# Optimization experiments

Hardware: AMD Instinct MI355X
Metric: run time of the kernel (lower is better)

The kernel has to match this reference:

```python
import jax, jax.numpy as jnp
import numpy as np

B, L, D, H, N, F_, DM = 16, 2048, 128, 4, 4, 129, 16
DK = D // H
DFF = 2 * D
INT = int(np.sqrt(D))  # 11
V = F_ + 1


def _uinit(key, shape, fan):
    s = float(np.sqrt(6.0 / fan))
    return jax.random.uniform(key, shape, jnp.float32, -s, s)


def setup_inputs() -> dict:
    key = jax.random.key(0)
    ks = jax.random.split(key, 24)
    return {
        "values": jax.random.normal(ks[0], (B, L), jnp.float32),
        "times": jax.random.uniform(ks[1], (B, L), jnp.float32),
        "variables": jax.random.randint(ks[2], (B, L), 0, F_),
        "input_mask": jax.random.randint(ks[3], (B, L), 0, 2).astype(bool),
        "demographics": jax.random.normal(ks[4], (B, DM), jnp.float32),
        # CVE time
        "W1t": _uinit(ks[5], (1, INT), 1 + INT), "b1t": jnp.zeros((INT,), jnp.float32),
        "W2t": _uinit(ks[6], (INT, D), INT + D),
        # CVE value
        "W1v": _uinit(ks[7], (1, INT), 1 + INT), "b1v": jnp.zeros((INT,), jnp.float32),
        "W2v": _uinit(ks[8], (INT, D), INT + D),
        # variable embedding table
        "var_table": jax.random.normal(ks[9], (V, D), jnp.float32),
        # transformer stacks (init_proj: uniform(-s, s), s = sqrt(6/(fan_in+fan_out)) of last two dims)
        "Wq": _uinit(ks[10], (N, H, D, DK), D + DK),
        "Wk": _uinit(ks[11], (N, H, D, DK), D + DK),
        "Wv": _uinit(ks[12], (N, H, D, DK), D + DK),
        "Wo": _uinit(ks[13], (N, D, D), 2 * D),
        "W1": _uinit(ks[14], (N, D, DFF), D + DFF), "b1": jnp.zeros((N, 1, 1, DFF), jnp.float32),
        "W2": _uinit(ks[15], (N, DFF, D), DFF + D), "b2": jnp.zeros((N, 1, 1, D), jnp.float32),
        # fusion attention
        "Wf": _uinit(ks[16], (D, D), 2 * D), "bf": jnp.zeros((D,), jnp.float32),
        "uf": _uinit(ks[17], (D, 1), D + 1),
        # demographics MLP
        "Wd1": _uinit(ks[18], (DM, 2 * D), DM + 2 * D), "bd1": jnp.zeros((2 * D,), jnp.float32),
        "Wd2": _uinit(ks[19], (2 * D, D), 3 * D), "bd2": jnp.zeros((D,), jnp.float32),
        # head: forecast_fc
        "Wh": _uinit(ks[20], (2 * D, F_), 2 * D + F_), "bh": jnp.zeros((F_,), jnp.float32),
    }


def reference(values, times, variables, input_mask, demographics,
              W1t, b1t, W2t, W1v, b1v, W2v, var_table,
              Wq, Wk, Wv, Wo, W1, b1, W2, b2,
              Wf, bf, uf, Wd1, bd1, Wd2, bd2, Wh, bh):
    FMIN = jnp.finfo(values.dtype).min
    # demographics MLP
    demo = jnp.tanh(demographics @ Wd1 + bd1) @ Wd2 + bd2
    # continuous value embeddings (CVE): x -> tanh(x*W1 + b1) @ W2
    te = jnp.tanh(times[..., None] * W1t[0] + b1t) @ W2t    # [B,L,D]
    ve = jnp.tanh(values[..., None] * W1v[0] + b1v) @ W2v   # [B,L,D]
    x = te + ve + var_table[variables]                      # [B,L,D]
    # additive pairwise mask (finite FMIN, matches torch finfo.min semantics)
    m = input_mask
    pair = m[:, :, None] & m[:, None, :]                    # [B,L,L]
    addm = jnp.where(pair[:, None, :, :], 0.0, FMIN)        # [B,1,L,L]
    n_layers = Wq.shape[0]
    bsz, max_len, _ = x.shape
    for i in range(n_layers):
        q = jnp.einsum('bld,hde->bhle', x, Wq[i])
        k = jnp.einsum('bld,hde->bhle', x, Wk[i])
        v = jnp.einsum('bld,hde->bhle', x, Wv[i])
        A = jnp.einsum('bhle,bhke->bhlk', q, k) + addm      # NOTE: no 1/sqrt(dk) scaling, as in source
        A = jax.nn.softmax(A, axis=-1)
        o = jnp.einsum('bhlk,bhke->blhe', A, v).reshape(bsz, max_len, -1)
        x = o @ Wo[i] + x
        f = jax.nn.gelu(x @ W1[i] + b1[i], approximate=False)
        x = f @ W2[i] + b2[i] + x
    # fusion attention pooling
    att = (jnp.tanh(x @ Wf + bf) @ uf)[:, :, 0]             # [B,L]
    att = att + jnp.where(m, 0.0, FMIN)
    w = jax.nn.softmax(att, axis=-1)
    ts = jnp.sum(x * w[:, :, None], axis=1)                 # [B,D]
    emb = jnp.concatenate([ts, demo], axis=-1)              # [B,2D]
    return emb @ Wh + bh                                    # [B,features_num]
```

## Files before the change

### kernel.cpp

```cpp
#include <hip/hip_runtime.h>
#include <hip/hip_bf16.h>
#include <math.h>

#define B_   16
#define L_   2048
#define D_   128
#define H_   4
#define NL_  4
#define DK_  32
#define DFF_ 256
#define INTD_ 11
#define F_OUT 129
#define DM_  16
#define FMINV (-3.402823466e38f)
#define LOG2E 1.4426950408889634f

#define BL_  (B_*L_)
#define SZ_X (BL_*D_)

#define WT_Q 0
#define WT_K 16384
#define WT_V 32768
#define WT_O 49152
#define WT_1 65536
#define WT_2 98304
#define WT_TOT 131072

typedef __attribute__((ext_vector_type(8))) short bf16x8;
typedef __attribute__((ext_vector_type(4))) float f32x4;

#if __has_builtin(__builtin_amdgcn_exp2f)
#define EXP2F(x) __builtin_amdgcn_exp2f(x)
#else
#define EXP2F(x) __expf(0.69314718055994531f*(x))
#endif

static __device__ __forceinline__ short f2bf(float x) {
    union { __hip_bfloat16 h; short s; } u;
    u.h = __float2bfloat16(x);
    return u.s;
}
static __device__ __forceinline__ float bf2f(short s) {
    union { __hip_bfloat16 h; short t; } u;
    u.t = s;
    return __bfloat162float(u.h);
}
static __device__ __forceinline__ void split2(float v, short& h, short& l) {
    h = f2bf(v); l = f2bf(v - bf2f(h));
}
static __device__ __forceinline__ void split_trunc(float v, short& h, short& l) {
    unsigned u = __float_as_uint(v);
    h = (short)(u >> 16);
    float r = v - __uint_as_float(u & 0xffff0000u);
    l = (short)(__float_as_uint(r) >> 16);
}

__global__ __launch_bounds__(256)
void compact_kernel(const int* __restrict__ mask, int* __restrict__ pos,
                    int* __restrict__ kcount, float* __restrict__ cfm,
                    float* __restrict__ x)
{
    int b = blockIdx.x, t = threadIdx.x;
    int lane = t & 63, w = t >> 6;
    __shared__ int wsum[4];
    __shared__ int tot_s;
    int mv[8], loc[8], s = 0;
#pragma unroll
    for (int i = 0; i < 8; ++i) {
        mv[i] = mask[b*L_ + t*8 + i];
        loc[i] = s;
        s += mv[i];
    }
    int v = s;
#pragma unroll
    for (int d = 1; d < 64; d <<= 1) {
        int y = __shfl_up(v, d);
        if (lane >= d) v += y;
    }
    int excl = v - s;
    if (lane == 63) wsum[w] = v;
    __syncthreads();
    int wbase = 0;
    for (int i = 0; i < w; ++i) wbase += wsum[i];
    int base = wbase + excl;
#pragma unroll
    for (int i = 0; i < 8; ++i)
        pos[b*L_ + t*8 + i] = mv[i] ? (base + loc[i]) : -1;
    if (t == 255) { kcount[b] = base + s; tot_s = base + s; }
    __syncthreads();
    int tot = tot_s;
    for (int l = t; l < L_; l += 256) cfm[b*L_ + l] = (l < tot) ? 0.0f : FMINV;
    int end = (tot + 63) & ~63;
    int nz = (end - tot) * D_;
    for (int i = t; i < nz; i += 256)
        x[((size_t)(b*2048 + tot))*D_ + i] = 0.0f;
}

__global__ __launch_bounds__(128)
void embed_kernel(const float* __restrict__ values, const float* __restrict__ times,
                  const int* __restrict__ variables, const int* __restrict__ pos,
                  const float* __restrict__ W1t, const float* __restrict__ b1t,
                  const float* __restrict__ W2t,
                  const float* __restrict__ W1v, const float* __restrict__ b1v,
                  const float* __restrict__ W2v,
                  const float* __restrict__ var_table, float* __restrict__ x)
{
    int bl = blockIdx.x;
// ... 101 lines not shown
#pragma unroll
        for (int j = 0; j < 2; ++j) {
            size_t wi = (size_t)(32*w + 16*j + m)*D_ + 32*ks + 8*qd;
            wh[j] = *(const bf16x8*)(Wh + wi);
            wl[j] = *(const bf16x8*)(Wl + wi);
        }
#pragma unroll
        for (int r4 = 0; r4 < 4; ++r4) {
            bf16x8 ah = *(const bf16x8*)&Ahi[(16*r4 + m)*136 + 32*ks + 8*qd];
            bf16x8 al = *(const bf16x8*)&Alo[(16*r4 + m)*136 + 32*ks + 8*qd];
#pragma unroll
            for (int j = 0; j < 2; ++j) {
                acc[r4][j] = __builtin_amdgcn_mfma_f32_16x16x32_bf16(wh[j], ah, acc[r4][j], 0, 0, 0);
                acc[r4][j] = __builtin_amdgcn_mfma_f32_16x16x32_bf16(wh[j], al, acc[r4][j], 0, 0, 0);
                acc[r4][j] = __builtin_amdgcn_mfma_f32_16x16x32_bf16(wl[j], ah, acc[r4][j], 0, 0, 0);
            }
        }
    }

#pragma unroll
    for (int r4 = 0; r4 < 4; ++r4) {
        int row = row0 + 16*r4 + m;
        int l = row & 2047;
#pragma unroll
        for (int j = 0; j < 2; ++j) {
            int col = 32*w + 16*j + 4*qd;
            f32x4 v = acc[r4][j];
            if (sec == 0) {
                float4 sv = {v[0], v[1], v[2], v[3]};
                *(float4*)(qout + (size_t)row*D_ + col) = sv;
            } else if (sec == 1) {
                size_t idx = ((size_t)((bb*4 + w)*2048 + l))*32 + (col & 31);
                short4 hi4, lo4;
                split2(v[0], hi4.x, lo4.x);
                split2(v[1], hi4.y, lo4.y);
                split2(v[2], hi4.z, lo4.z);
                split2(v[3], hi4.w, lo4.w);
                *(short4*)(khi + idx) = hi4;
                *(short4*)(klo + idx) = lo4;
            } else {
                size_t basep = (size_t)(bb*4 + w)*32;
#pragma unroll
                for (int e = 0; e < 4; ++e) {
                    int d = 16*j + 4*qd + e;
                    short hh, ll; split2(v[e], hh, ll);
                    vhiT[(basep + d)*2048 + l] = hh;
                    vloT[(basep + d)*2048 + l] = ll;
                }
            }
        }
    }
}

__global__ __launch_bounds__(256)
void attn_mfma_kernel(const float* __restrict__ q,
                      const short* __restrict__ khi, const short* __restrict__ klo,
                      const short* __restrict__ vhiT, const short* __restrict__ vloT,
                      const int* __restrict__ kcount, const float* __restrict__ cfm,
                      float* __restrict__ opart, float* __restrict__ mlm,
                      float* __restrict__ mll)
{
    (void)cfm;
    __shared__ short KhiS[2][2048];
    __shared__ short KloS[2][2048];
    __shared__ short Vthi[2][2048];
    __shared__ short Vtlo[2][2048];
    __shared__ short Ps[4][1024];

    const int t    = threadIdx.x;
    const int w    = t >> 6;
    const int lane = t & 63;
    const int m    = lane & 15;
    const int qd   = lane >> 4;
    const int qt = blockIdx.x, b = blockIdx.z;
    const int h = blockIdx.y & 3, half = blockIdx.y >> 2;

    const int Kb = kcount[b];
    if (qt*64 >= Kb) return;
    const int nt = (Kb + 63) >> 6;
    const int ntH = (nt + 1) >> 1;
    const int kt0 = half * ntH;
    const int kt1 = (kt0 + ntH < nt) ? (kt0 + ntH) : nt;
    const size_t mlbase = (((size_t)(b*4 + h))*2 + half)*2048;

    if (kt0 >= kt1) {
        if (lane < 16) {
            mlm[mlbase + qt*64 + 16*w + lane] = FMINV;
            mll[mlbase + qt*64 + 16*w + lane] = 0.0f;
        }
        return;
    }

    const size_t hd = ((size_t)(b*4 + h))*2048*32;
    const int vd = t >> 3;
    const int vk = t & 7;
    const size_t vbase = ((size_t)(b*4 + h)*32 + vd)*2048 + vk*8;
    const int vw_off = vd*64 + ((vk ^ (vd & 7)) << 3);

    const int qrow = qt*64 + 16*w + m;
    const float* qp = q + ((size_t)(b*L_ + qrow))*D_ + h*DK_ + 8*qd;
    float qf[8];
    *(float4*)&qf[0] = *(const float4*)qp;
    *(float4*)&qf[4] = *(const float4*)(qp + 4);
    bf16x8 qhi, qlo;
#pragma unroll
    for (int j = 0; j < 8; ++j) {
        float qs = qf[j] * LOG2E;
        short hs = f2bf(qs);
        qhi[j] = hs;
        qlo[j] = f2bf(qs - bf2f(hs));
    }

    bf16x8 pkh, pkl, pvh, pvl;
    {
        const size_t gk = hd + (size_t)kt0*64*32 + t*8;
        pkh = *(const bf16x8*)(khi + gk);
        pkl = *(const bf16x8*)(klo + gk);
        pvh = *(const bf16x8*)(vhiT + vbase + (size_t)kt0*64);
        pvl = *(const bf16x8*)(vloT + vbase + (size_t)kt0*64);
    }

    float m_old = -INFINITY, l_run = 0.0f;
    f32x4 o_acc[2] = {{0,0,0,0},{0,0,0,0}};

    for (int kt = kt0; kt < kt1; ++kt) {
        const int buf = kt & 1;
        *(bf16x8*)&KhiS[buf][t*8] = pkh;
        *(bf16x8*)&KloS[buf][t*8] = pkl;
        *(bf16x8*)&Vthi[buf][vw_off] = pvh;
        *(bf16x8*)&Vtlo[buf][vw_off] = pvl;
        if (kt + 1 < kt1) {
            const size_t gk = hd + (size_t)(kt+1)*64*32 + t*8;
            pkh = *(const bf16x8*)(khi + gk);
            pkl = *(const bf16x8*)(klo + gk);
            pvh = *(const bf16x8*)(vhiT + vbase + (size_t)(kt+1)*64);
            pvl = *(const bf16x8*)(vloT + vbase + (size_t)(kt+1)*64);
        }
        asm volatile("s_waitcnt lgkmcnt(0)" ::: "memory");
        __builtin_amdgcn_s_barrier();
        __builtin_amdgcn_sched_barrier(0);

        f32x4 sf[4];
#pragma unroll
        for (int k4 = 0; k4 < 4; ++k4) {
            bf16x8 ka = *(const bf16x8*)&KhiS[buf][(16*k4 + m)*32 + 8*qd];
            bf16x8 kl = *(const bf16x8*)&KloS[buf][(16*k4 + m)*32 + 8*qd];
            f32x4 c = {0,0,0,0};
            c = __builtin_amdgcn_mfma_f32_16x16x32_bf16(ka, qhi, c, 0, 0, 0);
            c = __builtin_amdgcn_mfma_f32_16x16x32_bf16(ka, qlo, c, 0, 0, 0);
            c = __builtin_amdgcn_mfma_f32_16x16x32_bf16(kl, qhi, c, 0, 0, 0);
            sf[k4] = c;
        }

        float sv[16];
        if (kt == nt - 1) {
            const int rel = Kb - kt*64;
#pragma unroll
            for (int k4 = 0; k4 < 4; ++k4)
#pragma unroll
                for (int e = 0; e < 4; ++e)
                    sv[4*k4+e] = sf[k4][e] +
                        (((16*k4 + 4*qd + e) < rel) ? 0.0f : FMINV);
        } else {
#pragma unroll
            for (int k4 = 0; k4 < 4; ++k4)
#pragma unroll
                for (int e = 0; e < 4; ++e)
                    sv[4*k4+e] = sf[k4][e];
        }

        float mx8[8];
#pragma unroll
        for (int j = 0; j < 8; ++j) mx8[j] = fmaxf(sv[2*j], sv[2*j+1]);
#pragma unroll
        for (int j = 0; j < 4; ++j) mx8[j] = fmaxf(mx8[j], mx8[j+4]);
        float tmax = fmaxf(fmaxf(mx8[0], mx8[1]), fmaxf(mx8[2], mx8[3]));
        tmax = fmaxf(tmax, __shfl_xor(tmax, 16));
        tmax = fmaxf(tmax, __shfl_xor(tmax, 32));
        float mnew  = fmaxf(m_old, tmax);
        float alpha = EXP2F(m_old - mnew);
        float pj[16];
        short pbh[16], pbl[16];
#pragma unroll
        for (int j = 0; j < 16; ++j) {
            float p = EXP2F(sv[j] - mnew);
            pj[j] = p;
            split_trunc(p, pbh[j], pbl[j]);
        }
        float ps8[8];
#pragma unroll
        for (int j = 0; j < 8; ++j) ps8[j] = pj[2*j] + pj[2*j+1];
#pragma unroll
        for (int j = 0; j < 4; ++j) ps8[j] = ps8[j] + ps8[j+4];
        float psum = (ps8[0] + ps8[1]) + (ps8[2] + ps8[3]);
        psum += __shfl_xor(psum, 16);
        psum += __shfl_xor(psum, 32);
        l_run = l_run * alpha + psum;
        m_old = mnew;

#pragma unroll
        for (int k4 = 0; k4 < 4; ++k4) {
            short4 s4h;
            s4h.x = pbh[4*k4+0]; s4h.y = pbh[4*k4+1]; s4h.z = pbh[4*k4+2]; s4h.w = pbh[4*k4+3];
            int chunk = 2*k4 + (qd >> 1);
            int po = m*64 + ((chunk ^ (m & 7)) << 3) + ((qd & 1) << 2);
            *(short4*)&Ps[w][po] = s4h;
        }

        {
            float a0 = __shfl(alpha, 4*qd + 0);
            float a1 = __shfl(alpha, 4*qd + 1);
            float a2 = __shfl(alpha, 4*qd + 2);
            float a3 = __shfl(alpha, 4*qd + 3);
            o_acc[0][0]*=a0; o_acc[0][1]*=a1; o_acc[0][2]*=a2; o_acc[0][3]*=a3;
            o_acc[1][0]*=a0; o_acc[1][1]*=a1; o_acc[1][2]*=a2; o_acc[1][3]*=a3;
        }
#pragma unroll
        for (int s = 0; s < 2; ++s) {
#pragma unroll
            for (int tp = 0; tp < 2; ++tp) {
                bf16x8 pah = *(const bf16x8*)&Ps[w][m*64 + (((4*s + qd) ^ (m & 7)) << 3)];
                int vr = (16*tp + m)*64 + (((4*s + qd) ^ (m & 7)) << 3);
                bf16x8 vh = *(const bf16x8*)&Vthi[buf][vr];
                bf16x8 vl = *(const bf16x8*)&Vtlo[buf][vr];
                o_acc[tp] = __builtin_amdgcn_mfma_f32_16x16x32_bf16(pah, vh, o_acc[tp], 0, 0, 0);
                o_acc[tp] = __builtin_amdgcn_mfma_f32_16x16x32_bf16(pah, vl, o_acc[tp], 0, 0, 0);
            }
        }
#pragma unroll
        for (int k4 = 0; k4 < 4; ++k4) {
            short4 s4l;
            s4l.x = pbl[4*k4+0]; s4l.y = pbl[4*k4+1]; s4l.z = pbl[4*k4+2]; s4l.w = pbl[4*k4+3];
            int chunk = 2*k4 + (qd >> 1);
            int po = m*64 + ((chunk ^ (m & 7)) << 3) + ((qd & 1) << 2);
            *(short4*)&Ps[w][po] = s4l;
        }
#pragma unroll
        for (int s = 0; s < 2; ++s) {
#pragma unroll
            for (int tp = 0; tp < 2; ++tp) {
                bf16x8 pal = *(const bf16x8*)&Ps[w][m*64 + (((4*s + qd) ^ (m & 7)) << 3)];
                int vr = (16*tp + m)*64 + (((4*s + qd) ^ (m & 7)) << 3);
                bf16x8 vh = *(const bf16x8*)&Vthi[buf][vr];
                o_acc[tp] = __builtin_amdgcn_mfma_f32_16x16x32_bf16(pal, vh, o_acc[tp], 0, 0, 0);
            }
        }
    }

    if (lane < 16) {
        mlm[mlbase + qt*64 + 16*w + lane] = m_old;
        mll[mlbase + qt*64 + 16*w + lane] = l_run;
    }
    float* ob = opart + (size_t)half*SZ_X;
#pragma unroll
    for (int tp = 0; tp < 2; ++tp)
#pragma unroll
        for (int r = 0; r < 4; ++r)
            ob[((size_t)(b*L_ + qt*64 + 16*w + 4*qd + r))*D_ + h*DK_ + 16*tp + m] =
                o_acc[tp][r];
}

__global__ __launch_bounds__(256)
void wo_ffn1_kernel(const float* __restrict__ opart, const float* __restrict__ mlm,
                    const float* __restrict__ mll,
                    const short* __restrict__ WhiO, const short* __restrict__ WloO,
                    const short* __restrict__ Whi1, const short* __restrict__ Wlo1,
                    const float* __restrict__ b1,
                    const int* __restrict__ kcount, float* __restrict__ x,
                    float* __restrict__ hb)
{
    const int row0 = blockIdx.x * 64;
    const int bb = row0 >> 11;
    if ((row0 & 2047) >= ((kcount[bb] + 63) & ~63)) return;

    __shared__ short Ahi[64*136];
    __shared__ short Alo[64*136];
    const int t = threadIdx.x;
    const int w = t >> 6, lane = t & 63;
    const int m = lane & 15, qd = lane >> 4;

#pragma unroll
    for (int i = 0; i < 8; ++i) {
        int r = (t >> 5) + 8*i;
        int c = (t & 31) * 4;
        int row = row0 + r;
        int l = row & 2047;
        int h = c >> 5;
        size_t i0 = (((size_t)(bb*4 + h))*2 + 0)*2048 + l;
        size_t i1 = i0 + 2048;
        float m0 = mlm[i0], m1 = mlm[i1];
        float l0 = mll[i0], l1 = mll[i1];
        float M  = fmaxf(m0, m1);
        float w0 = EXP2F(m0 - M), w1 = EXP2F(m1 - M);
        float inv = 1.0f / (l0*w0 + l1*w1);
        float s0 = w0 * inv, s1 = w1 * inv;
        float4 o0 = *(const float4*)(opart + (size_t)row*D_ + c);
        float4 o1 = *(const float4*)(opart + (size_t)(BL_ + row)*D_ + c);
        float4 av;
        av.x = s0*o0.x + s1*o1.x;
        av.y = s0*o0.y + s1*o1.y;
        av.z = s0*o0.z + s1*o1.z;
        av.w = s0*o0.w + s1*o1.w;
        short4 hi4, lo4;
        split2(av.x, hi4.x, lo4.x);
        split2(av.y, hi4.y, lo4.y);
        split2(av.z, hi4.z, lo4.z);
        split2(av.w, hi4.w, lo4.w);
        *(short4*)&Ahi[r*136 + c] = hi4;
        *(short4*)&Alo[r*136 + c] = lo4;
    }
    __syncthreads();

    f32x4 acc[4][2];
#pragma unroll
    for (int r4 = 0; r4 < 4; ++r4)
#pragma unroll
        for (int j = 0; j < 2; ++j) acc[r4][j] = (f32x4){0,0,0,0};
#pragma unroll
    for (int ks = 0; ks < 4; ++ks) {
        bf16x8 wh[2], wl[2];
#pragma unroll
        for (int j = 0; j < 2; ++j) {
            size_t wi = (size_t)(32*w + 16*j + m)*D_ + 32*ks + 8*qd;
            wh[j] = *(const bf16x8*)(WhiO + wi);
            wl[j] = *(const bf16x8*)(WloO + wi);
        }
#pragma unroll
        for (int r4 = 0; r4 < 4; ++r4) {
            bf16x8 ah = *(const bf16x8*)&Ahi[(16*r4 + m)*136 + 32*ks + 8*qd];
            bf16x8 al = *(const bf16x8*)&Alo[(16*r4 + m)*136 + 32*ks + 8*qd];
#pragma unroll
            for (int j = 0; j < 2; ++j) {
                acc[r4][j] = __builtin_amdgcn_mfma_f32_16x16x32_bf16(wh[j], ah, acc[r4][j], 0, 0, 0);
                acc[r4][j] = __builtin_amdgcn_mfma_f32_16x16x32_bf16(wh[j], al, acc[r4][j], 0, 0, 0);
                acc[r4][j] = __builtin_amdgcn_mfma_f32_16x16x32_bf16(wl[j], ah, acc[r4][j], 0, 0, 0);
            }
        }
    }

#pragma unroll
    for (int r4 = 0; r4 < 4; ++r4) {
        int row = row0 + 16*r4 + m;
#pragma unroll
        for (int j = 0; j < 2; ++j) {
            int col = 32*w + 16*j + 4*qd;
            float4 rv = *(const float4*)(x + (size_t)row*D_ + col);
            acc[r4][j][0] += rv.x; acc[r4][j][1] += rv.y;
            acc[r4][j][2] += rv.z; acc[r4][j][3] += rv.w;
            float4 sv = {acc[r4][j][0], acc[r4][j][1], acc[r4][j][2], acc[r4][j][3]};
            *(float4*)(x + (size_t)row*D_ + col) = sv;
        }
    }
    __syncthreads();

#pragma unroll
    for (int r4 = 0; r4 < 4; ++r4) {
#pragma unroll
        for (int j = 0; j < 2; ++j) {
            int col = 32*w + 16*j + 4*qd;
            short4 hi4, lo4;
            split2(acc[r4][j][0], hi4.x, lo4.x);
            split2(acc[r4][j][1], hi4.y, lo4.y);
            split2(acc[r4][j][2], hi4.z, lo4.z);
            split2(acc[r4][j][3], hi4.w, lo4.w);
            *(short4*)&Ahi[(16*r4 + m)*136 + col] = hi4;
            *(short4*)&Alo[(16*r4 + m)*136 + col] = lo4;
        }
    }
    __syncthreads();

    f32x4 a2[4][4];
#pragma unroll
    for (int r4 = 0; r4 < 4; ++r4)
#pragma unroll
        for (int jj = 0; jj < 4; ++jj) a2[r4][jj] = (f32x4){0,0,0,0};
#pragma unroll
    for (int ks = 0; ks < 4; ++ks) {
        bf16x8 wh[4], wl[4];
#pragma unroll
        for (int jj = 0; jj < 4; ++jj) {
            size_t wi = (size_t)(64*w + 16*jj + m)*D_ + 32*ks + 8*qd;
            wh[jj] = *(const bf16x8*)(Whi1 + wi);
            wl[jj] = *(const bf16x8*)(Wlo1 + wi);
        }
#pragma unroll
        for (int r4 = 0; r4 < 4; ++r4) {
            bf16x8 ah = *(const bf16x8*)&Ahi[(16*r4 + m)*136 + 32*ks + 8*qd];
            bf16x8 al = *(const bf16x8*)&Alo[(16*r4 + m)*136 + 32*ks + 8*qd];
#pragma unroll
            for (int jj = 0; jj < 4; ++jj) {
                a2[r4][jj] = __builtin_amdgcn_mfma_f32_16x16x32_bf16(wh[jj], ah, a2[r4][jj], 0, 0, 0);
                a2[r4][jj] = __builtin_amdgcn_mfma_f32_16x16x32_bf16(wh[jj], al, a2[r4][jj], 0, 0, 0);
                a2[r4][jj] = __builtin_amdgcn_mfma_f32_16x16x32_bf16(wl[jj], ah, a2[r4][jj], 0, 0, 0);
            }
        }
    }

#pragma unroll
    for (int r4 = 0; r4 < 4; ++r4) {
        int row = row0 + 16*r4 + m;
#pragma unroll
        for (int jj = 0; jj < 4; ++jj) {
            int col = 64*w + 16*jj + 4*qd;
            f32x4 v = a2[r4][jj];
            float4 bv = *(const float4*)(b1 + col);
            v[0] += bv.x; v[1] += bv.y; v[2] += bv.z; v[3] += bv.w;
#pragma unroll
            for (int e = 0; e < 4; ++e)
                v[e] = 0.5f * v[e] * (1.0f + erff(v[e] * 0.70710678118654752f));
            float4 sv = {v[0], v[1], v[2], v[3]};
            *(float4*)(hb + (size_t)row*DFF_ + col) = sv;
        }
    }
}

template<int TAIL>
__global__ __launch_bounds__(256)
void ffn2_next_kernel(const float* __restrict__ hb,
                      const short* __restrict__ Whi2, const short* __restrict__ Wlo2,
                      const float* __restrict__ b2,
                      const short* __restrict__ WhiN, const short* __restrict__ WloN,
                      const float* __restrict__ bfv, const float* __restrict__ uf,
                      const float* __restrict__ cfm,
                      const int* __restrict__ kcount, float* __restrict__ x,
                      float* __restrict__ qout,
                      short* __restrict__ khi, short* __restrict__ klo,
                      short* __restrict__ vhiT, short* __restrict__ vloT,
                      float* __restrict__ attb)
{
    const int row0 = blockIdx.x * 64;
    const int bb = row0 >> 11;
    if ((row0 & 2047) >= ((kcount[bb] + 63) & ~63)) return;

    __shared__ short Ahi[64*136];
    __shared__ short Alo[64*136];
    __shared__ float part[64][16];
    const int t = threadIdx.x;
    const int w = t >> 6, lane = t & 63;
    const int m = lane & 15, qd = lane >> 4;

    f32x4 acc[4][2];
#pragma unroll
    for (int r4 = 0; r4 < 4; ++r4)
#pragma unroll
        for (int j = 0; j < 2; ++j) acc[r4][j] = (f32x4){0,0,0,0};

    for (int kb = 0; kb < DFF_; kb += 128) {
        if (kb) __syncthreads();
#pragma unroll
        for (int i = 0; i < 8; ++i) {
            int r = (t >> 5) + 8*i;
            int c = (t & 31) * 4;
            float4 av = *(const float4*)(hb + (size_t)(row0 + r)*DFF_ + kb + c);
            short4 hi4, lo4;
            split2(av.x, hi4.x, lo4.x);
            split2(av.y, hi4.y, lo4.y);
            split2(av.z, hi4.z, lo4.z);
            split2(av.w, hi4.w, lo4.w);
            *(short4*)&Ahi[r*136 + c] = hi4;
            *(short4*)&Alo[r*136 + c] = lo4;
        }
        __syncthreads();

#pragma unroll
        for (int ks = 0; ks < 4; ++ks) {
            bf16x8 wh[2], wl[2];
#pragma unroll
            for (int j = 0; j < 2; ++j) {
                size_t wi = (size_t)(32*w + 16*j + m)*DFF_ + kb + 32*ks + 8*qd;
                wh[j] = *(const bf16x8*)(Whi2 + wi);
                wl[j] = *(const bf16x8*)(Wlo2 + wi);
            }
#pragma unroll
            for (int r4 = 0; r4 < 4; ++r4) {
                bf16x8 ah = *(const bf16x8*)&Ahi[(16*r4 + m)*136 + 32*ks + 8*qd];
                bf16x8 al = *(const bf16x8*)&Alo[(16*r4 + m)*136 + 32*ks + 8*qd];
#pragma unroll
                for (int j = 0; j < 2; ++j) {
                    acc[r4][j] = __builtin_amdgcn_mfma_f32_16x16x32_bf16(wh[j], ah, acc[r4][j], 0, 0, 0);
                    acc[r4][j] = __builtin_amdgcn_mfma_f32_16x16x32_bf16(wh[j], al, acc[r4][j], 0, 0, 0);
                    acc[r4][j] = __builtin_amdgcn_mfma_f32_16x16x32_bf16(wl[j], ah, acc[r4][j], 0, 0, 0);
                }
            }
        }
    }

#pragma unroll
    for (int r4 = 0; r4 < 4; ++r4) {
        int row = row0 + 16*r4 + m;
#pragma unroll
        for (int j = 0; j < 2; ++j) {
            int col = 32*w + 16*j + 4*qd;
            float4 bv = *(const float4*)(b2 + col);
            float4 rv = *(const float4*)(x + (size_t)row*D_ + col);
            acc[r4][j][0] += bv.x + rv.x; acc[r4][j][1] += bv.y + rv.y;
            acc[r4][j][2] += bv.z + rv.z; acc[r4][j][3] += bv.w + rv.w;
            float4 sv = {acc[r4][j][0], acc[r4][j][1], acc[r4][j][2], acc[r4][j][3]};
            *(float4*)(x + (size_t)row*D_ + col) = sv;
        }
    }
    __syncthreads();

#pragma unroll
    for (int r4 = 0; r4 < 4; ++r4) {
#pragma unroll
        for (int j = 0; j < 2; ++j) {
            int col = 32*w + 16*j + 4*qd;
            short4 hi4, lo4;
            split2(acc[r4][j][0], hi4.x, lo4.x);
            split2(acc[r4][j][1], hi4.y, lo4.y);
            split2(acc[r4][j][2], hi4.z, lo4.z);
            split2(acc[r4][j][3], hi4.w, lo4.w);
            *(short4*)&Ahi[(16*r4 + m)*136 + col] = hi4;
            *(short4*)&Alo[(16*r4 + m)*136 + col] = lo4;
        }
    }
    __syncthreads();

    if (TAIL == 0) {
#pragma unroll
        for (int sec = 0; sec < 3; ++sec) {
            const short* Wh = WhiN + sec*16384;
            const short* Wl = WloN + sec*16384;
            f32x4 a3[4][2];
#pragma unroll
            for (int r4 = 0; r4 < 4; ++r4)
#pragma unroll
                for (int j = 0; j < 2; ++j) a3[r4][j] = (f32x4){0,0,0,0};
#pragma unroll
            for (int ks = 0; ks < 4; ++ks) {
                bf16x8 wh[2], wl[2];
#pragma unroll
                for (int j = 0; j < 2; ++j) {
                    size_t wi = (size_t)(32*w + 16*j + m)*D_ + 32*ks + 8*qd;
                    wh[j] = *(const bf16x8*)(Wh + wi);
                    wl[j] = *(const bf16x8*)(Wl + wi);
                }
#pragma unroll
                for (int r4 = 0; r4 < 4; ++r4) {
                    bf16x8 ah = *(const bf16x8*)&Ahi[(16*r4 + m)*136 + 32*ks + 8*qd];
                    bf16x8 al = *(const bf16x8*)&Alo[(16*r4 + m)*136 + 32*ks + 8*qd];
#pragma unroll
                    for (int j = 0; j < 2; ++j) {
                        a3[r4][j] = __builtin_amdgcn_mfma_f32_16x16x32_bf16(wh[j], ah, a3[r4][j], 0, 0, 0);
                        a3[r4][j] = __builtin_amdgcn_mfma_f32_16x16x32_bf16(wh[j], al, a3[r4][j], 0, 0, 0);
                        a3[r4][j] = __builtin_amdgcn_mfma_f32_16x16x32_bf16(wl[j], ah, a3[r4][j], 0, 0, 0);
                    }
                }
            }
#pragma unroll
            for (int r4 = 0; r4 < 4; ++r4) {
                int row = row0 + 16*r4 + m;
                int l = row & 2047;
#pragma unroll
                for (int j = 0; j < 2; ++j) {
                    int col = 32*w + 16*j + 4*qd;
                    f32x4 v = a3[r4][j];
                    if (sec == 0) {
                        float4 sv = {v[0], v[1], v[2], v[3]};
                        *(float4*)(qout + (size_t)row*D_ + col) = sv;
                    } else if (sec == 1) {
                        size_t idx = ((size_t)((bb*4 + w)*2048 + l))*32 + (col & 31);
                        short4 hi4, lo4;
                        split2(v[0], hi4.x, lo4.x);
                        split2(v[1], hi4.y, lo4.y);
                        split2(v[2], hi4.z, lo4.z);
                        split2(v[3], hi4.w, lo4.w);
                        *(short4*)(khi + idx) = hi4;
                        *(short4*)(klo + idx) = lo4;
                    } else {
// ... 151 lines not shown
                              hipStream_t stream)
{
    (void)in_sizes; (void)n_in; (void)out_size; (void)ws_size;
    const float* values       = (const float*)d_in[0];
    const float* times        = (const float*)d_in[1];
    const int*   variables    = (const int*)  d_in[2];
    const int*   input_mask   = (const int*)  d_in[3];
    const float* demographics = (const float*)d_in[4];
    const float* W1t = (const float*)d_in[5];
    const float* b1t = (const float*)d_in[6];
    const float* W2t = (const float*)d_in[7];
    const float* W1v = (const float*)d_in[8];
    const float* b1v = (const float*)d_in[9];
    const float* W2v = (const float*)d_in[10];
    const float* var_table = (const float*)d_in[11];
    const float* Wq  = (const float*)d_in[12];
    const float* Wk  = (const float*)d_in[13];
    const float* Wv  = (const float*)d_in[14];
    const float* Wo  = (const float*)d_in[15];
    const float* W1  = (const float*)d_in[16];
    const float* b1  = (const float*)d_in[17];
    const float* W2  = (const float*)d_in[18];
    const float* b2  = (const float*)d_in[19];
    const float* Wf  = (const float*)d_in[20];
    const float* bfv = (const float*)d_in[21];
    const float* uf  = (const float*)d_in[22];
    const float* Wd1 = (const float*)d_in[23];
    const float* bd1 = (const float*)d_in[24];
    const float* Wd2 = (const float*)d_in[25];
    const float* bd2 = (const float*)d_in[26];
    const float* Wh  = (const float*)d_in[27];
    const float* bhv = (const float*)d_in[28];
    float* out = (float*)d_out;

    float* ws     = (float*)d_ws;
    float* x      = ws;
    float* qb     = ws + (size_t)SZ_X;
    float* region = ws + (size_t)2*SZ_X;
    short* khi    = (short*)region;
    short* klo    = khi + (size_t)SZ_X;
    short* vhiT   = klo + (size_t)SZ_X;
    short* vloT   = vhiT + (size_t)SZ_X;
    float* attb   = ws + (size_t)4*SZ_X;
    float* attp   = attb + BL_;
    float* partb  = attp + BL_;
    short* wt_hi  = (short*)(partb + B_*16*D_);
    short* wt_lo  = wt_hi + ((size_t)NL_*WT_TOT + 16384);
    int*   posb   = (int*)(wt_lo + ((size_t)NL_*WT_TOT + 16384));
    int*   kcountb= posb + BL_;
    float* cfmb   = (float*)(kcountb + B_ + 3);
    float* opart  = cfmb + BL_;
    float* mlm    = opart + (size_t)2*SZ_X;
    float* mll    = mlm + (size_t)B_*H_*2*2048;
    float* hb     = mll + (size_t)B_*H_*2*2048;
    short* wfhi   = wt_hi + (size_t)NL_*WT_TOT;
    short* wflo   = wt_lo + (size_t)NL_*WT_TOT;

    compact_kernel<<<B_, 256, 0, stream>>>(input_mask, posb, kcountb, cfmb, x);
    embed_kernel<<<BL_, 128, 0, stream>>>(values, times, variables, posb,
                                          W1t, b1t, W2t, W1v, b1v, W2v,
                                          var_table, x);
    split_all_kernel<<<(NL_*131072 + 16384)/256, 256, 0, stream>>>(
        Wq, Wk, Wv, Wo, W1, W2, Wf, wt_hi, wt_lo);

    gemm_qkv_fused<<<dim3(BL_/64, 3), 256, 0, stream>>>(x,
        wt_hi + 0*WT_TOT, wt_lo + 0*WT_TOT, kcountb, qb, khi, klo, vhiT, vloT);

    for (int i = 0; i < NL_; ++i) {
        short* whL = wt_hi + (size_t)i*WT_TOT;
        short* wlL = wt_lo + (size_t)i*WT_TOT;
        attn_mfma_kernel<<<dim3(L_/64, H_*2, B_), 256, 0, stream>>>(qb, khi, klo,
            vhiT, vloT, kcountb, cfmb, opart, mlm, mll);
        wo_ffn1_kernel<<<BL_/64, 256, 0, stream>>>(opart, mlm, mll,
            whL+WT_O, wlL+WT_O, whL+WT_1, wlL+WT_1, b1 + i*DFF_,
            kcountb, x, hb);
        if (i < NL_ - 1) {
            short* whN = wt_hi + (size_t)(i+1)*WT_TOT;
            short* wlN = wt_lo + (size_t)(i+1)*WT_TOT;
            ffn2_next_kernel<0><<<BL_/64, 256, 0, stream>>>(hb,
                whL+WT_2, wlL+WT_2, b2 + i*D_, whN, wlN,
                nullptr, nullptr, nullptr, kcountb, x,
                qb, khi, klo, vhiT, vloT, nullptr);
        } else {
            ffn2_next_kernel<1><<<BL_/64, 256, 0, stream>>>(hb,
                whL+WT_2, wlL+WT_2, b2 + i*D_, wfhi, wflo,
                bfv, uf, cfmb, kcountb, x,
                nullptr, nullptr, nullptr, nullptr, nullptr, attb);
        }
    }

    pool_stats_kernel<<<B_, 256, 0, stream>>>(attb, kcountb, attp);
    pool_partial_kernel<<<dim3(16, B_), 128, 0, stream>>>(attp, x, partb);
    head_kernel<<<B_, 256, 0, stream>>>(partb, demographics, Wd1, bd1, Wd2, bd2,
                                        Wh, bhv, out);
}
```

Measured before the change: 781.8 us.

## Single-buffer attention K/V LDS tiles and raise occupancy hint

The attention kernel drops the double-buffered K/V shared-memory tiles for single buffers, adding a barrier before each tile store. Its launch bounds now request 6 blocks per CU, so less LDS per block and a register cap should allow more resident waves to hide latency. The P fragment load is hoisted out of the inner tp loop, and several __syncthreads are replaced with an explicit LDS-wait plus s_barrier helper. The extra barrier per K tile and possible register spilling under the tighter occupancy bound could offset the gain.

```diff
diff --git a/kernel.cpp b/kernel.cpp
--- a/kernel.cpp
+++ b/kernel.cpp
@@ -53,6 +53,10 @@
     h = (short)(u >> 16);
     float r = v - __uint_as_float(u & 0xffff0000u);
     l = (short)(__float_as_uint(r) >> 16);
+}
+static __device__ __forceinline__ void bar_lgkm() {
+    asm volatile("s_waitcnt lgkmcnt(0)" ::: "memory");
+    __builtin_amdgcn_s_barrier();
 }
 
 __global__ __launch_bounds__(256)
@@ -260,7 +264,7 @@
     }
 }
 
-__global__ __launch_bounds__(256)
+__global__ __launch_bounds__(256, 6)
 void attn_mfma_kernel(const float* __restrict__ q,
                       const short* __restrict__ khi, const short* __restrict__ klo,
                       const short* __restrict__ vhiT, const short* __restrict__ vloT,
@@ -269,10 +273,10 @@
                       float* __restrict__ mll)
 {
     (void)cfm;
-    __shared__ short KhiS[2][2048];
-    __shared__ short KloS[2][2048];
-    __shared__ short Vthi[2][2048];
-    __shared__ short Vtlo[2][2048];
+    __shared__ short KhiS[2048];
+    __shared__ short KloS[2048];
+    __shared__ short Vthi[2048];
+    __shared__ short Vtlo[2048];
     __shared__ short Ps[4][1024];
 
     const int t    = threadIdx.x;
@@ -332,11 +336,11 @@
     f32x4 o_acc[2] = {{0,0,0,0},{0,0,0,0}};
 
     for (int kt = kt0; kt < kt1; ++kt) {
-        const int buf = kt & 1;
-        *(bf16x8*)&KhiS[buf][t*8] = pkh;
-        *(bf16x8*)&KloS[buf][t*8] = pkl;
-        *(bf16x8*)&Vthi[buf][vw_off] = pvh;
-        *(bf16x8*)&Vtlo[buf][vw_off] = pvl;
+        bar_lgkm();
+        *(bf16x8*)&KhiS[t*8] = pkh;
+        *(bf16x8*)&KloS[t*8] = pkl;
+        *(bf16x8*)&Vthi[vw_off] = pvh;
+        *(bf16x8*)&Vtlo[vw_off] = pvl;
         if (kt + 1 < kt1) {
             const size_t gk = hd + (size_t)(kt+1)*64*32 + t*8;
             pkh = *(const bf16x8*)(khi + gk);
@@ -344,15 +348,14 @@
             pvh = *(const bf16x8*)(vhiT + vbase + (size_t)(kt+1)*64);
             pvl = *(const bf16x8*)(vloT + vbase + (size_t)(kt+1)*64);
         }
-        asm volatile("s_waitcnt lgkmcnt(0)" ::: "memory");
-        __builtin_amdgcn_s_barrier();
+        bar_lgkm();
         __builtin_amdgcn_sched_barrier(0);
 
         f32x4 sf[4];
 #pragma unroll
         for (int k4 = 0; k4 < 4; ++k4) {
-            bf16x8 ka = *(const bf16x8*)&KhiS[buf][(16*k4 + m)*32 + 8*qd];
-            bf16x8 kl = *(const bf16x8*)&KloS[buf][(16*k4 + m)*32 + 8*qd];
+            bf16x8 ka = *(const bf16x8*)&KhiS[(16*k4 + m)*32 + 8*qd];
+            bf16x8 kl = *(const bf16x8*)&KloS[(16*k4 + m)*32 + 8*qd];
             f32x4 c = {0,0,0,0};
             c = __builtin_amdgcn_mfma_f32_16x16x32_bf16(ka, qhi, c, 0, 0, 0);
             c = __builtin_amdgcn_mfma_f32_16x16x32_bf16(ka, qlo, c, 0, 0, 0);
@@ -425,12 +428,12 @@
         }
 #pragma unroll
         for (int s = 0; s < 2; ++s) {
+            bf16x8 pah = *(const bf16x8*)&Ps[w][m*64 + (((4*s + qd) ^ (m & 7)) << 3)];
 #pragma unroll
             for (int tp = 0; tp < 2; ++tp) {
-                bf16x8 pah = *(const bf16x8*)&Ps[w][m*64 + (((4*s + qd) ^ (m & 7)) << 3)];
                 int vr = (16*tp + m)*64 + (((4*s + qd) ^ (m & 7)) << 3);
-                bf16x8 vh = *(const bf16x8*)&Vthi[buf][vr];
-                bf16x8 vl = *(const bf16x8*)&Vtlo[buf][vr];
+                bf16x8 vh = *(const bf16x8*)&Vthi[vr];
+                bf16x8 vl = *(const bf16x8*)&Vtlo[vr];
                 o_acc[tp] = __builtin_amdgcn_mfma_f32_16x16x32_bf16(pah, vh, o_acc[tp], 0, 0, 0);
                 o_acc[tp] = __builtin_amdgcn_mfma_f32_16x16x32_bf16(pah, vl, o_acc[tp], 0, 0, 0);
             }
@@ -445,11 +448,11 @@
         }
 #pragma unroll
         for (int s = 0; s < 2; ++s) {
+            bf16x8 pal = *(const bf16x8*)&Ps[w][m*64 + (((4*s + qd) ^ (m & 7)) << 3)];
 #pragma unroll
             for (int tp = 0; tp < 2; ++tp) {
-                bf16x8 pal = *(const bf16x8*)&Ps[w][m*64 + (((4*s + qd) ^ (m & 7)) << 3)];
                 int vr = (16*tp + m)*64 + (((4*s + qd) ^ (m & 7)) << 3);
-                bf16x8 vh = *(const bf16x8*)&Vthi[buf][vr];
+                bf16x8 vh = *(const bf16x8*)&Vthi[vr];
                 o_acc[tp] = __builtin_amdgcn_mfma_f32_16x16x32_bf16(pal, vh, o_acc[tp], 0, 0, 0);
             }
         }
@@ -559,7 +562,7 @@
             *(float4*)(x + (size_t)row*D_ + col) = sv;
         }
     }
-    __syncthreads();
+    bar_lgkm();
 
 #pragma unroll
     for (int r4 = 0; r4 < 4; ++r4) {
@@ -575,7 +578,7 @@
             *(short4*)&Alo[(16*r4 + m)*136 + col] = lo4;
         }
     }
-    __syncthreads();
+    bar_lgkm();
 
     f32x4 a2[4][4];
 #pragma unroll
@@ -654,7 +657,7 @@
         for (int j = 0; j < 2; ++j) acc[r4][j] = (f32x4){0,0,0,0};
 
     for (int kb = 0; kb < DFF_; kb += 128) {
-        if (kb) __syncthreads();
+        if (kb) bar_lgkm();
 #pragma unroll
         for (int i = 0; i < 8; ++i) {
             int r = (t >> 5) + 8*i;
@@ -707,7 +710,7 @@
             *(float4*)(x + (size_t)row*D_ + col) = sv;
         }
     }
-    __syncthreads();
+    bar_lgkm();
 
 #pragma unroll
     for (int r4 = 0; r4 < 4; ++r4) {
@@ -723,7 +726,7 @@
             *(short4*)&Alo[(16*r4 + m)*136 + col] = lo4;
         }
     }
-    __syncthreads();
+    bar_lgkm();
 
     if (TAIL == 0) {
 #pragma unroll
```

Result: slower. 1.168 ms (+49.4%).

## Fuse Wo, FFN1 and FFN2 into one per-layer kernel, keeping hidden activations on-chip

Applied to the files above, without the earlier changes.

Merges the Wo+FFN1 kernel and the FFN2+next-QKV kernel into a single layer kernel. The 256-wide GELU hidden activation is produced in two 128-column halves, split to bf16 hi/lo in shared memory and immediately consumed by the FFN2 GEMM. The intermediate global buffer hb and one launch per layer go away, as does the intermediate write/read of x. The cost is more register pressure (xnew, acc2 and a2 are all live), extra barriers, and restaging x into shared memory after the first half.

```diff
diff --git a/kernel.cpp b/kernel.cpp
--- a/kernel.cpp
+++ b/kernel.cpp
@@ -53,6 +53,10 @@
     h = (short)(u >> 16);
     float r = v - __uint_as_float(u & 0xffff0000u);
     l = (short)(__float_as_uint(r) >> 16);
+}
+static __device__ __forceinline__ void bar_lgkm() {
+    asm volatile("s_waitcnt lgkmcnt(0)" ::: "memory");
+    __builtin_amdgcn_s_barrier();
 }
 
 __global__ __launch_bounds__(256)
@@ -344,8 +348,7 @@
             pvh = *(const bf16x8*)(vhiT + vbase + (size_t)(kt+1)*64);
             pvl = *(const bf16x8*)(vloT + vbase + (size_t)(kt+1)*64);
         }
-        asm volatile("s_waitcnt lgkmcnt(0)" ::: "memory");
-        __builtin_amdgcn_s_barrier();
+        bar_lgkm();
         __builtin_amdgcn_sched_barrier(0);
 
         f32x4 sf[4];
@@ -468,14 +471,23 @@
                 o_acc[tp][r];
 }
 
+template<int TAIL>
 __global__ __launch_bounds__(256)
-void wo_ffn1_kernel(const float* __restrict__ opart, const float* __restrict__ mlm,
-                    const float* __restrict__ mll,
-                    const short* __restrict__ WhiO, const short* __restrict__ WloO,
-                    const short* __restrict__ Whi1, const short* __restrict__ Wlo1,
-                    const float* __restrict__ b1,
-                    const int* __restrict__ kcount, float* __restrict__ x,
-                    float* __restrict__ hb)
+void layer_fused_kernel(const float* __restrict__ opart, const float* __restrict__ mlm,
+                        const float* __restrict__ mll,
+                        const short* __restrict__ WhiO, const short* __restrict__ WloO,
+                        const short* __restrict__ Whi1, const short* __restrict__ Wlo1,
+                        const float* __restrict__ b1,
+                        const short* __restrict__ Whi2, const short* __restrict__ Wlo2,
+                        const float* __restrict__ b2,
+                        const short* __restrict__ WhiN, const short* __restrict__ WloN,
+                        const float* __restrict__ bfv, const float* __restrict__ uf,
+                        const float* __restrict__ cfm,
+                        const int* __restrict__ kcount, float* __restrict__ x,
+                        float* __restrict__ qout,
+                        short* __restrict__ khi, short* __restrict__ klo,
+                        short* __restrict__ vhiT, short* __restrict__ vloT,
+                        float* __restrict__ attb)
 {
     const int row0 = blockIdx.x * 64;
     const int bb = row0 >> 11;
@@ -483,6 +495,7 @@
 
     __shared__ short Ahi[64*136];
     __shared__ short Alo[64*136];
+    __shared__ float part[64][16];
     const int t = threadIdx.x;
     const int w = t >> 6, lane = t & 63;
     const int m = lane & 15, qd = lane >> 4;
@@ -517,13 +530,13 @@
         *(short4*)&Ahi[r*136 + c] = hi4;
         *(short4*)&Alo[r*136 + c] = lo4;
     }
-    __syncthreads();
-
-    f32x4 acc[4][2];
+    bar_lgkm();
+
+    f32x4 xnew[4][2];
 #pragma unroll
     for (int r4 = 0; r4 < 4; ++r4)
 #pragma unroll
-        for (int j = 0; j < 2; ++j) acc[r4][j] = (f32x4){0,0,0,0};
+        for (int j = 0; j < 2; ++j) xnew[r4][j] = (f32x4){0,0,0,0};
 #pragma unroll
     for (int ks = 0; ks < 4; ++ks) {
         bf16x8 wh[2], wl[2];
@@ -539,13 +552,12 @@
             bf16x8 al = *(const bf16x8*)&Alo[(16*r4 + m)*136 + 32*ks + 8*qd];
 #pragma unroll
             for (int j = 0; j < 2; ++j) {
-                acc[r4][j] = __builtin_amdgcn_mfma_f32_16x16x32_bf16(wh[j], ah, acc[r4][j], 0, 0, 0);
-                acc[r4][j] = __builtin_amdgcn_mfma_f32_16x16x32_bf16(wh[j], al, acc[r4][j], 0, 0, 0);
-                acc[r4][j] = __builtin_amdgcn_mfma_f32_16x16x32_bf16(wl[j], ah, acc[r4][j], 0, 0, 0);
-            }
-        }
-    }
-
+                xnew[r4][j] = __builtin_amdgcn_mfma_f32_16x16x32_bf16(wh[j], ah, xnew[r4][j], 0, 0, 0);
+                xnew[r4][j] = __builtin_amdgcn_mfma_f32_16x16x32_bf16(wh[j], al, xnew[r4][j], 0, 0, 0);
+                xnew[r4][j] = __builtin_amdgcn_mfma_f32_16x16x32_bf16(wl[j], ah, xnew[r4][j], 0, 0, 0);
+            }
+        }
+    }
 #pragma unroll
     for (int r4 = 0; r4 < 4; ++r4) {
         int row = row0 + 16*r4 + m;
@@ -553,131 +565,48 @@
         for (int j = 0; j < 2; ++j) {
             int col = 32*w + 16*j + 4*qd;
             float4 rv = *(const float4*)(x + (size_t)row*D_ + col);
-            acc[r4][j][0] += rv.x; acc[r4][j][1] += rv.y;
-            acc[r4][j][2] += rv.z; acc[r4][j][3] += rv.w;
-            float4 sv = {acc[r4][j][0], acc[r4][j][1], acc[r4][j][2], acc[r4][j][3]};
-            *(float4*)(x + (size_t)row*D_ + col) = sv;
-        }
-    }
-    __syncthreads();
-
-#pragma unroll
-    for (int r4 = 0; r4 < 4; ++r4) {
+            xnew[r4][j][0] += rv.x; xnew[r4][j][1] += rv.y;
+            xnew[r4][j][2] += rv.z; xnew[r4][j][3] += rv.w;
+        }
+    }
+    bar_lgkm();
+
+#pragma unroll
+    for (int r4 = 0; r4 < 4; ++r4)
 #pragma unroll
         for (int j = 0; j < 2; ++j) {
             int col = 32*w + 16*j + 4*qd;
             short4 hi4, lo4;
-            split2(acc[r4][j][0], hi4.x, lo4.x);
-            split2(acc[r4][j][1], hi4.y, lo4.y);
-            split2(acc[r4][j][2], hi4.z, lo4.z);
-            split2(acc[r4][j][3], hi4.w, lo4.w);
+            split2(xnew[r4][j][0], hi4.x, lo4.x);
+            split2(xnew[r4][j][1], hi4.y, lo4.y);
+            split2(xnew[r4][j][2], hi4.z, lo4.z);
+            split2(xnew[r4][j][3], hi4.w, lo4.w);
             *(short4*)&Ahi[(16*r4 + m)*136 + col] = hi4;
             *(short4*)&Alo[(16*r4 + m)*136 + col] = lo4;
         }
-    }
-    __syncthreads();
-
-    f32x4 a2[4][4];
+    bar_lgkm();
+
+    f32x4 acc2[4][2];
 #pragma unroll
     for (int r4 = 0; r4 < 4; ++r4)
 #pragma unroll
-        for (int jj = 0; jj < 4; ++jj) a2[r4][jj] = (f32x4){0,0,0,0};
-#pragma unroll
-    for (int ks = 0; ks < 4; ++ks) {
-        bf16x8 wh[4], wl[4];
-#pragma unroll
-        for (int jj = 0; jj < 4; ++jj) {
-            size_t wi = (size_t)(64*w + 16*jj + m)*D_ + 32*ks + 8*qd;
-            wh[jj] = *(const bf16x8*)(Whi1 + wi);
-            wl[jj] = *(const bf16x8*)(Wlo1 + wi);
-        }
-#pragma unroll
-        for (int r4 = 0; r4 < 4; ++r4) {
-            bf16x8 ah = *(const bf16x8*)&Ahi[(16*r4 + m)*136 + 32*ks + 8*qd];
-            bf16x8 al = *(const bf16x8*)&Alo[(16*r4 + m)*136 + 32*ks + 8*qd];
-#pragma unroll
-            for (int jj = 0; jj < 4; ++jj) {
-                a2[r4][jj] = __builtin_amdgcn_mfma_f32_16x16x32_bf16(wh[jj], ah, a2[r4][jj], 0, 0, 0);
-                a2[r4][jj] = __builtin_amdgcn_mfma_f32_16x16x32_bf16(wh[jj], al, a2[r4][jj], 0, 0, 0);
-                a2[r4][jj] = __builtin_amdgcn_mfma_f32_16x16x32_bf16(wl[jj], ah, a2[r4][jj], 0, 0, 0);
-            }
-        }
-    }
-
-#pragma unroll
-    for (int r4 = 0; r4 < 4; ++r4) {
-        int row = row0 + 16*r4 + m;
-#pragma unroll
-        for (int jj = 0; jj < 4; ++jj) {
-            int col = 64*w + 16*jj + 4*qd;
-            f32x4 v = a2[r4][jj];
-            float4 bv = *(const float4*)(b1 + col);
-            v[0] += bv.x; v[1] += bv.y; v[2] += bv.z; v[3] += bv.w;
-#pragma unroll
-            for (int e = 0; e < 4; ++e)
-                v[e] = 0.5f * v[e] * (1.0f + erff(v[e] * 0.70710678118654752f));
-            float4 sv = {v[0], v[1], v[2], v[3]};
-            *(float4*)(hb + (size_t)row*DFF_ + col) = sv;
-        }
-    }
-}
-
-template<int TAIL>
-__global__ __launch_bounds__(256)
-void ffn2_next_kernel(const float* __restrict__ hb,
-                      const short* __restrict__ Whi2, const short* __restrict__ Wlo2,
-                      const float* __restrict__ b2,
-                      const short* __restrict__ WhiN, const short* __restrict__ WloN,
-                      const float* __restrict__ bfv, const float* __restrict__ uf,
-                      const float* __restrict__ cfm,
-                      const int* __restrict__ kcount, float* __restrict__ x,
-                      float* __restrict__ qout,
-                      short* __restrict__ khi, short* __restrict__ klo,
-                      short* __restrict__ vhiT, short* __restrict__ vloT,
-                      float* __restrict__ attb)
-{
-    const int row0 = blockIdx.x * 64;
-    const int bb = row0 >> 11;
-    if ((row0 & 2047) >= ((kcount[bb] + 63) & ~63)) return;
-
-    __shared__ short Ahi[64*136];
-    __shared__ short Alo[64*136];
-    __shared__ float part[64][16];
-    const int t = threadIdx.x;
-    const int w = t >> 6, lane = t & 63;
-    const int m = lane & 15, qd = lane >> 4;
-
-    f32x4 acc[4][2];
-#pragma unroll
-    for (int r4 = 0; r4 < 4; ++r4)
-#pragma unroll
-        for (int j = 0; j < 2; ++j) acc[r4][j] = (f32x4){0,0,0,0};
-
-    for (int kb = 0; kb < DFF_; kb += 128) {
-        if (kb) __syncthreads();
-#pragma unroll
-        for (int i = 0; i < 8; ++i) {
-            int r = (t >> 5) + 8*i;
-            int c = (t & 31) * 4;
-            float4 av = *(const float4*)(hb + (size_t)(row0 + r)*DFF_ + kb + c);
-            short4 hi4, lo4;
-            split2(av.x, hi4.x, lo4.x);
-            split2(av.y, hi4.y, lo4.y);
-            split2(av.z, hi4.z, lo4.z);
-            split2(av.w, hi4.w, lo4.w);
-            *(short4*)&Ahi[r*136 + c] = hi4;
-            *(short4*)&Alo[r*136 + c] = lo4;
-        }
-        __syncthreads();
-
+        for (int j = 0; j < 2; ++j) acc2[r4][j] = (f32x4){0,0,0,0};
+
+#pragma unroll
+    for (int half = 0; half < 2; ++half) {
+        f32x4 a2[4][2];
+#pragma unroll
+        for (int r4 = 0; r4 < 4; ++r4)
+#pragma unroll
+            for (int j = 0; j < 2; ++j) a2[r4][j] = (f32x4){0,0,0,0};
 #pragma unroll
         for (int ks = 0; ks < 4; ++ks) {
             bf16x8 wh[2], wl[2];
 #pragma unroll
             for (int j = 0; j < 2; ++j) {
-                size_t wi = (size_t)(32*w + 16*j + m)*DFF_ + kb + 32*ks + 8*qd;
-                wh[j] = *(const bf16x8*)(Whi2 + wi);
-                wl[j] = *(const bf16x8*)(Wlo2 + wi);
+                size_t wi = (size_t)(128*half + 32*w + 16*j + m)*D_ + 32*ks + 8*qd;
+                wh[j] = *(const bf16x8*)(Whi1 + wi);
+                wl[j] = *(const bf16x8*)(Wlo1 + wi);
             }
 #pragma unroll
             for (int r4 = 0; r4 < 4; ++r4) {
@@ -685,11 +614,77 @@
                 bf16x8 al = *(const bf16x8*)&Alo[(16*r4 + m)*136 + 32*ks + 8*qd];
 #pragma unroll
                 for (int j = 0; j < 2; ++j) {
-                    acc[r4][j] = __builtin_amdgcn_mfma_f32_16x16x32_bf16(wh[j], ah, acc[r4][j], 0, 0, 0);
-                    acc[r4][j] = __builtin_amdgcn_mfma_f32_16x16x32_bf16(wh[j], al, acc[r4][j], 0, 0, 0);
-                    acc[r4][j] = __builtin_amdgcn_mfma_f32_16x16x32_bf16(wl[j], ah, acc[r4][j], 0, 0, 0);
+                    a2[r4][j] = __builtin_amdgcn_mfma_f32_16x16x32_bf16(wh[j], ah, a2[r4][j], 0, 0, 0);
+                    a2[r4][j] = __builtin_amdgcn_mfma_f32_16x16x32_bf16(wh[j], al, a2[r4][j], 0, 0, 0);
+                    a2[r4][j] = __builtin_amdgcn_mfma_f32_16x16x32_bf16(wl[j], ah, a2[r4][j], 0, 0, 0);
                 }
             }
+        }
+#pragma unroll
+        for (int r4 = 0; r4 < 4; ++r4)
+#pragma unroll
+            for (int j = 0; j < 2; ++j) {
+                int col = 128*half + 32*w + 16*j + 4*qd;
+                float4 bv = *(const float4*)(b1 + col);
+                a2[r4][j][0] += bv.x; a2[r4][j][1] += bv.y;
+                a2[r4][j][2] += bv.z; a2[r4][j][3] += bv.w;
+#pragma unroll
+                for (int e = 0; e < 4; ++e)
+                    a2[r4][j][e] = 0.5f * a2[r4][j][e] *
+                                   (1.0f + erff(a2[r4][j][e] * 0.70710678118654752f));
+            }
+        bar_lgkm();
+#pragma unroll
+        for (int r4 = 0; r4 < 4; ++r4)
+#pragma unroll
+            for (int j = 0; j < 2; ++j) {
+                int lc = 32*w + 16*j + 4*qd;
+                short4 hi4, lo4;
+                split2(a2[r4][j][0], hi4.x, lo4.x);
+                split2(a2[r4][j][1], hi4.y, lo4.y);
+                split2(a2[r4][j][2], hi4.z, lo4.z);
+                split2(a2[r4][j][3], hi4.w, lo4.w);
+                *(short4*)&Ahi[(16*r4 + m)*136 + lc] = hi4;
+                *(short4*)&Alo[(16*r4 + m)*136 + lc] = lo4;
+            }
+        bar_lgkm();
+#pragma unroll
+        for (int ks = 0; ks < 4; ++ks) {
+            bf16x8 wh[2], wl[2];
+#pragma unroll
+            for (int j = 0; j < 2; ++j) {
+                size_t wi = (size_t)(32*w + 16*j + m)*DFF_ + 128*half + 32*ks + 8*qd;
+                wh[j] = *(const bf16x8*)(Whi2 + wi);
+                wl[j] = *(const bf16x8*)(Wlo2 + wi);
+            }
+#pragma unroll
+            for (int r4 = 0; r4 < 4; ++r4) {
+                bf16x8 ah = *(const bf16x8*)&Ahi[(16*r4 + m)*136 + 32*ks + 8*qd];
+                bf16x8 al = *(const bf16x8*)&Alo[(16*r4 + m)*136 + 32*ks + 8*qd];
+#pragma unroll
+                for (int j = 0; j < 2; ++j) {
+                    acc2[r4][j] = __builtin_amdgcn_mfma_f32_16x16x32_bf16(wh[j], ah, acc2[r4][j], 0, 0, 0);
+                    acc2[r4][j] = __builtin_amdgcn_mfma_f32_16x16x32_bf16(wh[j], al, acc2[r4][j], 0, 0, 0);
+                    acc2[r4][j] = __builtin_amdgcn_mfma_f32_16x16x32_bf16(wl[j], ah, acc2[r4][j], 0, 0, 0);
+                }
+            }
+        }
+        if (half == 0) {
+            bar_lgkm();
+#pragma unroll
+            for (int r4 = 0; r4 < 4; ++r4)
+#pragma unroll
+                for (int j = 0; j < 2; ++j) {
+                    int col = 32*w + 16*j + 4*qd;
+                    short4 hi4, lo4;
+                    split2(xnew[r4][j][0], hi4.x, lo4.x);
+                    split2(xnew[r4][j][1], hi4.y, lo4.y);
+                    split2(xnew[r4][j][2], hi4.z, lo4.z);
+                    split2(xnew[r4][j][3], hi4.w, lo4.w);
+                    *(short4*)&Ahi[(16*r4 + m)*136 + col] = hi4;
+                    *(short4*)&Alo[(16*r4 + m)*136 + col] = lo4;
+                }
+            bar_lgkm();
         }
     }
 
@@ -700,30 +695,30 @@
         for (int j = 0; j < 2; ++j) {
             int col = 32*w + 16*j + 4*qd;
             float4 bv = *(const float4*)(b2 + col);
-            float4 rv = *(const float4*)(x + (size_t)row*D_ + col);
-            acc[r4][j][0] += bv.x + rv.x; acc[r4][j][1] += bv.y + rv.y;
-            acc[r4][j][2] += bv.z + rv.z; acc[r4][j][3] += bv.w + rv.w;
-            float4 sv = {acc[r4][j][0], acc[r4][j][1], acc[r4][j][2], acc[r4][j][3]};
+            xnew[r4][j][0] += bv.x + acc2[r4][j][0];
+            xnew[r4][j][1] += bv.y + acc2[r4][j][1];
+            xnew[r4][j][2] += bv.z + acc2[r4][j][2];
+            xnew[r4][j][3] += bv.w + acc2[r4][j][3];
+            float4 sv = {xnew[r4][j][0], xnew[r4][j][1], xnew[r4][j][2], xnew[r4][j][3]};
             *(float4*)(x + (size_t)row*D_ + col) = sv;
         }
     }
-    __syncthreads();
-
-#pragma unroll
-    for (int r4 = 0; r4 < 4; ++r4) {
+    bar_lgkm();
+
+#pragma unroll
+    for (int r4 = 0; r4 < 4; ++r4)
 #pragma unroll
         for (int j = 0; j < 2; ++j) {
             int col = 32*w + 16*j + 4*qd;
             short4 hi4, lo4;
-            split2(acc[r4][j][0], hi4.x, lo4.x);
-            split2(acc[r4][j][1], hi4.y, lo4.y);
-            split2(acc[r4][j][2], hi4.z, lo4.z);
-            split2(acc[r4][j][3], hi4.w, lo4.w);
+            split2(xnew[r4][j][0], hi4.x, lo4.x);
+            split2(xnew[r4][j][1], hi4.y, lo4.y);
+            split2(xnew[r4][j][2], hi4.z, lo4.z);
+            split2(xnew[r4][j][3], hi4.w, lo4.w);
             *(short4*)&Ahi[(16*r4 + m)*136 + col] = hi4;
             *(short4*)&Alo[(16*r4 + m)*136 + col] = lo4;
         }
-    }
-    __syncthreads();
+    bar_lgkm();
 
     if (TAIL == 0) {
 #pragma unroll
@@ -981,7 +976,6 @@
     float* opart  = cfmb + BL_;
     float* mlm    = opart + (size_t)2*SZ_X;
     float* mll    = mlm + (size_t)B_*H_*2*2048;
-    float* hb     = mll + (size_t)B_*H_*2*2048;
     short* wfhi   = wt_hi + (size_t)NL_*WT_TOT;
     short* wflo   = wt_lo + (size_t)NL_*WT_TOT;
 
@@ -1000,18 +994,17 @@
         short* wlL = wt_lo + (size_t)i*WT_TOT;
         attn_mfma_kernel<<<dim3(L_/64, H_*2, B_), 256, 0, stream>>>(qb, khi, klo,
             vhiT, vloT, kcountb, cfmb, opart, mlm, mll);
-        wo_ffn1_kernel<<<BL_/64, 256, 0, stream>>>(opart, mlm, mll,
-            whL+WT_O, wlL+WT_O, whL+WT_1, wlL+WT_1, b1 + i*DFF_,
-            kcountb, x, hb);
         if (i < NL_ - 1) {
             short* whN = wt_hi + (size_t)(i+1)*WT_TOT;
             short* wlN = wt_lo + (size_t)(i+1)*WT_TOT;
-            ffn2_next_kernel<0><<<BL_/64, 256, 0, stream>>>(hb,
+            layer_fused_kernel<0><<<BL_/64, 256, 0, stream>>>(opart, mlm, mll,
+                whL+WT_O, wlL+WT_O, whL+WT_1, wlL+WT_1, b1 + i*DFF_,
                 whL+WT_2, wlL+WT_2, b2 + i*D_, whN, wlN,
                 nullptr, nullptr, nullptr, kcountb, x,
                 qb, khi, klo, vhiT, vloT, nullptr);
         } else {
-            ffn2_next_kernel<1><<<BL_/64, 256, 0, stream>>>(hb,
+            layer_fused_kernel<1><<<BL_/64, 256, 0, stream>>>(opart, mlm, mll,
+                whL+WT_O, wlL+WT_O, whL+WT_1, wlL+WT_1, b1 + i*DFF_,
                 whL+WT_2, wlL+WT_2, b2 + i*D_, wfhi, wflo,
                 bfv, uf, cfmb, kcountb, x,
                 nullptr, nullptr, nullptr, nullptr, nullptr, attb);
```

Result: slower. 803.4 us (+2.8%).
